# Optimization experiments

Measured on AMD Instinct MI355X. Metric: run time of the kernel, lower is better.

Reference implementation:

```python
import jax, jax.numpy as jnp
import numpy as np

N, C, H, W = 4, 256, 64, 64
K, G, PAD, STRIDE, DIL = 3, 8, 1, 1, 1
GC = C // G      # channels per group
P = K * K        # sampling points per group
HIN, WIN = H + 2 * PAD, W + 2 * PAD
BN_EPS = 1e-5
LN_EPS = 1e-5


def setup_inputs():
    key = jax.random.key(0)
    ks = jax.random.split(key, 8)
    f32 = jnp.float32
    return {
        "x": jax.random.normal(ks[0], (N, C, H, W), dtype=f32),
        "w_in": jax.random.normal(ks[1], (C, C), dtype=f32) * 0.05,
        "b_in": jnp.zeros((C,), f32),
        "w_dw": jax.random.normal(ks[2], (C, 1, K, K), dtype=f32) * 0.1,
        "b_dw": jnp.zeros((C,), f32),
        "ln_g": jnp.ones((C,), f32), "ln_b": jnp.zeros((C,), f32),
        "w_off": jax.random.normal(ks[3], (C, G * P * 2), dtype=f32) * 0.01,
        "b_off": jax.random.normal(ks[4], (G * P * 2,), dtype=f32) * 0.01,
        "w_mask": jax.random.normal(ks[5], (C, G * P), dtype=f32) * 0.01,
        "b_mask": jnp.zeros((G * P,), f32),
        "w_out": jax.random.normal(ks[6], (C, C), dtype=f32) * 0.05,
        "b_out": jnp.zeros((C,), f32),
        "bn_g": jnp.ones((C,), f32), "bn_b": jnp.zeros((C,), f32),
        "bn_mean": jnp.zeros((C,), f32), "bn_var": jnp.ones((C,), f32),
    }


def _bilinear(img, grid):
    # img: (B, Cc, Hh, Ww); grid: (B, S, P, 2) normalized to [-1,1],
    # matches F.grid_sample(mode='bilinear', padding_mode='zeros', align_corners=False)
    B, Cc, Hh, Ww = img.shape
    gx = (grid[..., 0] + 1.0) * 0.5 * Ww - 0.5
    gy = (grid[..., 1] + 1.0) * 0.5 * Hh - 0.5
    x0 = jnp.floor(gx)
    y0 = jnp.floor(gy)
    wx = gx - x0
    wy = gy - y0
    flat = img.reshape(B, Cc, Hh * Ww)

    def tap(xi, yi, wgt):
        valid = (xi >= 0) & (xi <= Ww - 1) & (yi >= 0) & (yi <= Hh - 1)
        idx = (jnp.clip(yi, 0, Hh - 1) * Ww + jnp.clip(xi, 0, Ww - 1)).astype(jnp.int32)
        v = jax.vmap(lambda im, ix: im[:, ix])(flat, idx)   # (B, Cc, S, P)
        return v * (wgt * valid.astype(img.dtype))[:, None]

    return (tap(x0, y0, (1 - wx) * (1 - wy)) + tap(x0 + 1, y0, wx * (1 - wy))
            + tap(x0, y0 + 1, (1 - wx) * wy) + tap(x0 + 1, y0 + 1, wx * wy))


def _forward(x, w_in, b_in, w_dw, b_dw, ln_g, ln_b, w_off, b_off,
             w_mask, b_mask, w_out, b_out, bn_g, bn_b, bn_mean, bn_var):
    xl = jnp.transpose(x, (0, 2, 3, 1))                      # (N,H,W,C) channels-last
    x_proj = xl @ w_in + b_in                                # input_proj
    # depthwise conv + LayerNorm + GELU feature branch for offset/mask prediction
    dw = jax.lax.conv_general_dilated(
        x, w_dw, (1, 1), ((PAD, PAD), (PAD, PAD)),
        feature_group_count=C, dimension_numbers=("NCHW", "OIHW", "NCHW"))
    dw = jnp.transpose(dw + b_dw[None, :, None, None], (0, 2, 3, 1))
    mu = dw.mean(-1, keepdims=True)
    var = ((dw - mu) ** 2).mean(-1, keepdims=True)
    dw = (dw - mu) * jax.lax.rsqrt(var + LN_EPS) * ln_g + ln_b
    x1 = jax.nn.gelu(dw, approximate=False)
    offset = x1 @ w_off + b_off                              # (N,H,W,G*P*2)
    mask = jax.nn.softmax((x1 @ w_mask + b_mask).reshape(N, H, W, G, P), axis=-1)
    # reference points + dilation kernel grid, normalized to padded input, (x,y) order
    ry = ((DIL * (K - 1)) // 2 + 0.5 + jnp.arange(H, dtype=x.dtype) * STRIDE) / HIN
    rx = ((DIL * (K - 1)) // 2 + 0.5 + jnp.arange(W, dtype=x.dtype) * STRIDE) / WIN
    ref = jnp.stack(jnp.broadcast_arrays(rx[None, :], ry[:, None]), axis=-1)  # (H,W,2)
    px = (jnp.arange(K, dtype=x.dtype) * DIL - (DIL * (K - 1)) // 2) / WIN
    py = (jnp.arange(K, dtype=x.dtype) * DIL - (DIL * (K - 1)) // 2) / HIN
    gx, gy = jnp.meshgrid(px, py, indexing="ij")             # kw-major flattening as in DCNv3
    kgrid = jnp.stack([gx, gy], -1).reshape(P, 2)
    norm = jnp.array([WIN, HIN], dtype=x.dtype)
    loc = (ref[None, :, :, None, None, :] + kgrid[None, None, None, None, :, :]
           + offset.reshape(N, H, W, G, P, 2) / norm)        # (N,H,W,G,P,2), offset_scale=1
    sgrid = 2.0 * loc - 1.0
    # group-split padded value tensor and deformable sampling
    xp = jnp.pad(x_proj, ((0, 0), (PAD, PAD), (PAD, PAD), (0, 0)))
    img = jnp.transpose(xp, (0, 3, 1, 2)).reshape(N * G, GC, HIN, WIN)
    sg = jnp.transpose(sgrid.reshape(N, H * W, G, P, 2), (0, 2, 1, 3, 4)).reshape(N * G, H * W, P, 2)
    sampled = _bilinear(img, sg)                             # (N*G, GC, H*W, P)
    m = jnp.transpose(mask.reshape(N, H * W, G, P), (0, 2, 1, 3)).reshape(N * G, 1, H * W, P)
    agg = (sampled * m).sum(-1)                              # (N*G, GC, H*W)
    y = jnp.transpose(agg.reshape(N, C, H * W), (0, 2, 1)).reshape(N, H, W, C)
    y = y @ w_out + b_out                                    # output_proj
    y = jnp.transpose(y, (0, 3, 1, 2))                       # back to NCHW
    y = (y - bn_mean[None, :, None, None]) * jax.lax.rsqrt(bn_var + BN_EPS)[None, :, None, None]
    y = y * bn_g[None, :, None, None] + bn_b[None, :, None, None]
    return y * jax.nn.sigmoid(y)                             # SiLU (Conv.default_act)


def reference(x, w_in, b_in, w_dw, b_dw, ln_g, ln_b, w_off, b_off,
              w_mask, b_mask, w_out, b_out, bn_g, bn_b, bn_mean, bn_var):
    return _forward(x, w_in, b_in, w_dw, b_dw, ln_g, ln_b, w_off, b_off,
                    w_mask, b_mask, w_out, b_out, bn_g, bn_b, bn_mean, bn_var)
```

## Files before the change

### kernel.cpp

```cpp
#include <hip/hip_runtime.h>
#include <math.h>

#define NB   4
#define CCH  256
#define HH   64
#define WW   64
#define GG   8
#define GCH  32
#define PP   9
#define HIN  66
#define WIN  66
#define HWSZ 4096
#define NPIX 16384

#define X16_ELEMS  (NPIX*CCH)
#define XP_ELEMS   (NB*HIN*WIN*CCH)
#define X1_ELEMS   (NPIX*CCH)
#define AGG_ELEMS  (NPIX*CCH)
#define WINT_ELEMS (CCH*CCH)
#define WOUTT_ELEMS (CCH*CCH)
#define WOMT_ELEMS (216*CCH)
#define OFF_ELEMS  (NPIX*144)
#define MSK_ELEMS  (NPIX*72)

typedef __attribute__((ext_vector_type(8))) short bf16x8;
typedef __attribute__((ext_vector_type(4))) float f32x4;

__device__ __forceinline__ unsigned short f2bf(float f) {
    unsigned int u = __float_as_uint(f);
    unsigned int r = (u + 0x7FFFu + ((u >> 16) & 1u)) >> 16;
    return (unsigned short)r;
}
__device__ __forceinline__ float bf2f(unsigned short s) {
    return __uint_as_float(((unsigned int)s) << 16);
}

#define SDW_STRIDE 258

__global__ __launch_bounds__(1024) void k_dw_prep(
    const float* __restrict__ x, const float* __restrict__ w_dw,
    const float* __restrict__ b_dw, const float* __restrict__ ln_g,
    const float* __restrict__ ln_b, const float* __restrict__ w_in,
    const float* __restrict__ w_off, const float* __restrict__ w_mask,
    const float* __restrict__ w_out, unsigned short* __restrict__ x1,
    unsigned short* __restrict__ x16, unsigned short* __restrict__ win_t,
    unsigned short* __restrict__ womt, unsigned short* __restrict__ wout_t,
    unsigned short* __restrict__ xp)
{
    const int b = blockIdx.x;
    const int tid = threadIdx.x;

    if (b >= 256) {
        const int gtid = (b - 256) * 1024 + tid;
        const int STRIDE = 34 * 1024;
        for (int i = gtid; i < 252928; i += STRIDE) {
            if (i < 65536) {
                int n = i & 255, k = i >> 8;
                win_t[n * 256 + k] = f2bf(w_in[i]);
            } else if (i < 131072) {
                int j = i - 65536;
                int n = j & 255, k = j >> 8;
                wout_t[n * 256 + k] = f2bf(w_out[j]);
            } else if (i < 186368) {
                int j = i - 131072;
                int k = j / 216, col = j - k * 216;
                float v = (col < 144) ? w_off[k * 144 + col]
                                      : w_mask[k * 72 + col - 144];
                womt[col * 256 + k] = f2bf(v);
            } else {
                int r = i - 186368;
                int seg = r >> 6, ln = r & 63;
                int n = seg / 260, rp = seg % 260;
                int h, w;
                if (rp < 66)       { h = 0;        w = rp; }
                else if (rp < 132) { h = 65;       w = rp - 66; }
                else if (rp < 196) { h = rp - 131; w = 0; }
                else               { h = rp - 195; w = 65; }
                uint2 z = make_uint2(0u, 0u);
                *(uint2*)&xp[(((size_t)n * HIN + h) * WIN + w) * CCH + ln * 4] = z;
            }
        }
        return;
    }

    __shared__ unsigned short sdw[64 * SDW_STRIDE];
    __shared__ unsigned short sxr[64 * SDW_STRIDE];
    __shared__ float r1s[16][64];
    __shared__ float r2s[16][64];
    __shared__ float mu_s[64];
    __shared__ float rs_s[64];

    const int h = b & 63;
    const int n = b >> 6;
    const int wave = tid >> 6;
    const int lane = tid & 63;

    const float* xn = x + (size_t)n * CCH * HWSZ;
    const bool h0ok = (h > 0);
    const bool h2ok = (h < HH - 1);

    float s1 = 0.f, s2 = 0.f;

#pragma unroll 4
    for (int it = 0; it < 16; it++) {
        const int c = it * 16 + wave;
        const float* xc = xn + (size_t)c * HWSZ + h * WW + lane;
        float v0 = h0ok ? xc[-WW] : 0.f;
        float v1 = xc[0];
        float v2 = h2ok ? xc[WW] : 0.f;

        const float* wk = w_dw + c * 9;
        float acc = b_dw[c];

        float l0 = __shfl_up(v0, 1);   if (lane == 0)  l0 = 0.f;
        float r0 = __shfl_down(v0, 1); if (lane == 63) r0 = 0.f;
        acc += wk[0] * l0 + wk[1] * v0 + wk[2] * r0;

        float l1 = __shfl_up(v1, 1);   if (lane == 0)  l1 = 0.f;
        float r1 = __shfl_down(v1, 1); if (lane == 63) r1 = 0.f;
        acc += wk[3] * l1 + wk[4] * v1 + wk[5] * r1;

        float l2 = __shfl_up(v2, 1);   if (lane == 0)  l2 = 0.f;
        float r2 = __shfl_down(v2, 1); if (lane == 63) r2 = 0.f;
        acc += wk[6] * l2 + wk[7] * v2 + wk[8] * r2;

        s1 += acc;
        s2 += acc * acc;
        sdw[lane * SDW_STRIDE + c] = f2bf(acc);
        sxr[lane * SDW_STRIDE + c] = f2bf(v1);
    }

    r1s[wave][lane] = s1;
    r2s[wave][lane] = s2;
    __syncthreads();

    if (tid < 64) {
        float a1 = 0.f, a2 = 0.f;
#pragma unroll
        for (int q = 0; q < 16; q++) { a1 += r1s[q][tid]; a2 += r2s[q][tid]; }
        float mu = a1 * (1.0f / 256.0f);
        float var = a2 * (1.0f / 256.0f) - mu * mu;
        mu_s[tid] = mu;
        rs_s[tid] = rsqrtf(var + 1e-5f);
    }
    __syncthreads();

    const int c0 = (tid & 63) * 4;
    const int wq = tid >> 6;
    float g4[4], b4[4];
#pragma unroll
    for (int i = 0; i < 4; i++) { g4[i] = ln_g[c0 + i]; b4[i] = ln_b[c0 + i]; }

    unsigned short* x1p  = x1  + (((size_t)n * HH + h) * WW) * CCH + c0;
    unsigned short* x16p = x16 + (((size_t)n * HH + h) * WW) * CCH + c0;
#pragma unroll
    for (int pass = 0; pass < 4; pass++) {
        int w = wq + pass * 16;
        float mu = mu_s[w], rs = rs_s[w];
        const unsigned short* row  = &sdw[w * SDW_STRIDE + c0];
        const unsigned short* rowx = &sxr[w * SDW_STRIDE + c0];
        unsigned short tmp[4];
#pragma unroll
        for (int i = 0; i < 4; i++) {
            float v = (bf2f(row[i]) - mu) * rs * g4[i] + b4[i];
            tmp[i] = f2bf(0.5f * v * (1.0f + erff(v * 0.70710678118654752f)));
        }
        ushort4 o; o.x = tmp[0]; o.y = tmp[1]; o.z = tmp[2]; o.w = tmp[3];
        *(ushort4*)&x1p[(size_t)w * CCH] = o;
        ushort4 xo; xo.x = rowx[0]; xo.y = rowx[1]; xo.z = rowx[2]; xo.w = rowx[3];
        *(ushort4*)&x16p[(size_t)w * CCH] = xo;
    }
}

__global__ __launch_bounds__(256) void k_proj(
    const unsigned short* __restrict__ x16, const unsigned short* __restrict__ win_t,
    const float* __restrict__ b_in, unsigned short* __restrict__ xp,
    const unsigned short* __restrict__ x1, const unsigned short* __restrict__ womt,
    const float* __restrict__ b_off, const float* __restrict__ b_mask,
    float* __restrict__ off, float* __restrict__ msk)
{
    const int b = blockIdx.x;
    const int tid = threadIdx.x;
    const int wave = tid >> 6;
    const int lane = tid & 63;
    const int r16  = lane & 15;
    const int quad = lane >> 4;
    const int mw   = wave * 32;

    f32x4 acc[2][4];
#pragma unroll
    for (int i = 0; i < 2; i++)
#pragma unroll
        for (int j = 0; j < 4; j++) acc[i][j] = (f32x4){0.f, 0.f, 0.f, 0.f};

    if (b < 512) {
        const int m0  = (b & 127) * 128;
        const int co0 = (b >> 7) * 64;
        const int n   = m0 >> 12;
        const int hw0 = m0 & 4095;

        const unsigned short* a0p = x16 + (size_t)(m0 + mw + r16) * CCH + quad * 8;
        const unsigned short* a1p = a0p + 16 * CCH;

#pragma unroll
        for (int k0 = 0; k0 < CCH; k0 += 32) {
            bf16x8 a0 = *(const bf16x8*)&a0p[k0];
            bf16x8 a1 = *(const bf16x8*)&a1p[k0];
#pragma unroll
            for (int nt = 0; nt < 4; nt++) {
                bf16x8 bfr = *(const bf16x8*)&win_t[(size_t)(co0 + nt * 16 + r16) * CCH + k0 + quad * 8];
                acc[0][nt] = __builtin_amdgcn_mfma_f32_16x16x32_bf16(a0, bfr, acc[0][nt], 0, 0, 0);
                acc[1][nt] = __builtin_amdgcn_mfma_f32_16x16x32_bf16(a1, bfr, acc[1][nt], 0, 0, 0);
            }
        }

#pragma unroll
        for (int nt = 0; nt < 4; nt++) {
            int co = co0 + nt * 16 + r16;
            float bias = b_in[co];
#pragma unroll
            for (int mt = 0; mt < 2; mt++) {
                int mbase = mw + mt * 16 + quad * 4;
#pragma unroll
                for (int r = 0; r < 4; r++) {
                    int hw = hw0 + mbase + r;
                    int h = hw >> 6, w = hw & 63;
                    xp[(((size_t)n * HIN + (h + 1)) * WIN + (w + 1)) * CCH + co] =
                        f2bf(acc[mt][nt][r] + bias);
                }
            }
        }
    } else {
        const int b2 = b - 512;
        const int m0  = (b2 & 127) * 128;
        const int co0 = (b2 >> 7) * 64;

        const unsigned short* a0p = x1 + (size_t)(m0 + mw + r16) * CCH + quad * 8;
        const unsigned short* a1p = a0p + 16 * CCH;

#pragma unroll
        for (int k0 = 0; k0 < CCH; k0 += 32) {
            bf16x8 a0 = *(const bf16x8*)&a0p[k0];
            bf16x8 a1 = *(const bf16x8*)&a1p[k0];
#pragma unroll
            for (int nt = 0; nt < 4; nt++) {
                int col = co0 + nt * 16 + r16;
                int colc = (col < 216) ? col : 215;
                bf16x8 bfr = *(const bf16x8*)&womt[(size_t)colc * CCH + k0 + quad * 8];
                acc[0][nt] = __builtin_amdgcn_mfma_f32_16x16x32_bf16(a0, bfr, acc[0][nt], 0, 0, 0);
                acc[1][nt] = __builtin_amdgcn_mfma_f32_16x16x32_bf16(a1, bfr, acc[1][nt], 0, 0, 0);
            }
        }

#pragma unroll
        for (int nt = 0; nt < 4; nt++) {
            int col = co0 + nt * 16 + r16;
            if (col >= 216) continue;
            float bias = (col < 144) ? b_off[col] : b_mask[col - 144];
#pragma unroll
            for (int mt = 0; mt < 2; mt++) {
                int mbase = m0 + mw + mt * 16 + quad * 4;
#pragma unroll
                for (int r = 0; r < 4; r++) {
                    int p = mbase + r;
                    float v = acc[mt][nt][r] + bias;
                    if (col < 144) off[(size_t)p * 144 + col] = v;
                    else           msk[(size_t)p * 72 + col - 144] = v;
                }
            }
        }
    }
}

__device__ __forceinline__ void acc8_tap(float* a, uint4 vv, float wgt) {
    a[0] += wgt * __uint_as_float(vv.x << 16);
    a[1] += wgt * __uint_as_float(vv.x & 0xffff0000u);
    a[2] += wgt * __uint_as_float(vv.y << 16);
    a[3] += wgt * __uint_as_float(vv.y & 0xffff0000u);
    a[4] += wgt * __uint_as_float(vv.z << 16);
    a[5] += wgt * __uint_as_float(vv.z & 0xffff0000u);
    a[6] += wgt * __uint_as_float(vv.w << 16);
    a[7] += wgt * __uint_as_float(vv.w & 0xffff0000u);
}

__global__ __launch_bounds__(256) void k_sample_agg(
    const unsigned short* __restrict__ xp, const float* __restrict__ off,
    const float* __restrict__ msk, unsigned short* __restrict__ agg)
{
    __shared__ float  sm[576];
    __shared__ int2   tco[576];
    __shared__ float4 twt[576];

    const int tid = threadIdx.x;
    const int s0 = blockIdx.x * 8;

    if (tid < 64) {
        const int pix = tid >> 3, g = tid & 7;
        const float* mskp = msk + (size_t)(s0 + pix) * 72 + g * 9;
        float e[9];
        float mx = -1e30f;
#pragma unroll
        for (int p = 0; p < PP; p++) { e[p] = mskp[p]; mx = fmaxf(mx, e[p]); }
        float sum = 0.f;
#pragma unroll
        for (int p = 0; p < PP; p++) { e[p] = __expf(e[p] - mx); sum += e[p]; }
        float rs = 1.0f / sum;
#pragma unroll
        for (int p = 0; p < PP; p++) sm[tid * 9 + p] = e[p] * rs;
    }
    __syncthreads();

    for (int idx = tid; idx < 576; idx += 256) {
        int pix = idx / 72;
        int rem = idx - pix * 72;
        int g = rem / 9;
        int p = rem - g * 9;
        int s = s0 + pix;
        int hw = s & 4095;
        int h = hw >> 6, w = hw & 63;
        const float* offp = off + (size_t)s * 144 + g * 18 + p * 2;
        float ox = offp[0], oy = offp[1];
        int i = p / 3, j = p - i * 3;
        float fx = (float)(w + i) + ox;
        float fy = (float)(h + j) + oy;
        float x0f = floorf(fx), y0f = floorf(fy);
        int x0 = (int)x0f, y0 = (int)y0f;
        float wx = fx - x0f, wy = fy - y0f;
        float m = sm[idx];
        float w00 = (1.f - wx) * (1.f - wy) * m;
        float w10 = wx * (1.f - wy) * m;
        float w01 = (1.f - wx) * wy * m;
        float w11 = wx * wy * m;
        int x1c = x0 + 1, y1c = y0 + 1;
        if (!((x0  >= 0) && (x0  < WIN))) { w00 = 0.f; w01 = 0.f; }
        if (!((x1c >= 0) && (x1c < WIN))) { w10 = 0.f; w11 = 0.f; }
        if (!((y0  >= 0) && (y0  < HIN))) { w00 = 0.f; w10 = 0.f; }
        if (!((y1c >= 0) && (y1c < HIN))) { w01 = 0.f; w11 = 0.f; }
        int cx0 = min(max(x0, 0), WIN - 1), cx1 = min(max(x1c, 0), WIN - 1);
        int cy0 = min(max(y0, 0), HIN - 1), cy1 = min(max(y1c, 0), HIN - 1);
        tco[idx] = make_int2(cx0 | (cx1 << 16), cy0 | (cy1 << 16));
        twt[idx] = make_float4(w00, w10, w01, w11);
    }
    __syncthreads();

    const int pix = tid >> 5;
    const int l5 = tid & 31;
    const int g = l5 >> 2, c8 = l5 & 3;
    const int s = s0 + pix;
    const int n = s >> 12;
    const unsigned short* base = xp + (size_t)n * HIN * WIN * CCH + g * GCH + c8 * 8;
    const int tbase = pix * 72 + g * 9;

    float a[8];
#pragma unroll
    for (int i = 0; i < 8; i++) a[i] = 0.f;

#pragma unroll
    for (int p = 0; p < PP; p++) {
        int2 cc = tco[tbase + p];
        float4 wt = twt[tbase + p];
        int cx0 = cc.x & 0xFFFF, cx1 = cc.x >> 16;
        int cy0 = cc.y & 0xFFFF, cy1 = cc.y >> 16;
        const unsigned short* r0 = base + (size_t)(cy0 * WIN) * CCH;
        const unsigned short* r1 = base + (size_t)(cy1 * WIN) * CCH;
        uint4 v00 = *(const uint4*)&r0[(size_t)cx0 * CCH];
        uint4 v10 = *(const uint4*)&r0[(size_t)cx1 * CCH];
        uint4 v01 = *(const uint4*)&r1[(size_t)cx0 * CCH];
        uint4 v11 = *(const uint4*)&r1[(size_t)cx1 * CCH];
        acc8_tap(a, v00, wt.x);
        acc8_tap(a, v10, wt.y);
        acc8_tap(a, v01, wt.z);
        acc8_tap(a, v11, wt.w);
    }

    uint4 o;
    o.x = (unsigned int)f2bf(a[0]) | ((unsigned int)f2bf(a[1]) << 16);
    o.y = (unsigned int)f2bf(a[2]) | ((unsigned int)f2bf(a[3]) << 16);
    o.z = (unsigned int)f2bf(a[4]) | ((unsigned int)f2bf(a[5]) << 16);
    o.w = (unsigned int)f2bf(a[6]) | ((unsigned int)f2bf(a[7]) << 16);
    *(uint4*)&agg[(size_t)s * CCH + g * GCH + c8 * 8] = o;
}

__global__ __launch_bounds__(256) void k_gemm_out(
    const unsigned short* __restrict__ agg, const unsigned short* __restrict__ wout_t,
    const float* __restrict__ b_out, const float* __restrict__ bn_g,
    const float* __restrict__ bn_b, const float* __restrict__ bn_mean,
    const float* __restrict__ bn_var, float* __restrict__ out)
{
    const int m0  = blockIdx.x * 128;
    const int co0 = blockIdx.y * 64;
    const int tid = threadIdx.x;
    const int n   = m0 >> 12;
    const int hw0 = m0 & 4095;

    const int wave = tid >> 6;
    const int lane = tid & 63;
    const int r16  = lane & 15;
    const int quad = lane >> 4;
    const int mw   = wave * 32;

    f32x4 acc[2][4];
#pragma unroll
    for (int i = 0; i < 2; i++)
#pragma unroll
        for (int j = 0; j < 4; j++) acc[i][j] = (f32x4){0.f, 0.f, 0.f, 0.f};

    const unsigned short* a0p = agg + (size_t)(m0 + mw + r16) * CCH + quad * 8;
    const unsigned short* a1p = a0p + 16 * CCH;

#pragma unroll
    for (int k0 = 0; k0 < CCH; k0 += 32) {
        bf16x8 a0 = *(const bf16x8*)&a0p[k0];
        bf16x8 a1 = *(const bf16x8*)&a1p[k0];
#pragma unroll
        for (int nt = 0; nt < 4; nt++) {
            bf16x8 bfr = *(const bf16x8*)&wout_t[(size_t)(co0 + nt * 16 + r16) * CCH + k0 + quad * 8];
            acc[0][nt] = __builtin_amdgcn_mfma_f32_16x16x32_bf16(a0, bfr, acc[0][nt], 0, 0, 0);
            acc[1][nt] = __builtin_amdgcn_mfma_f32_16x16x32_bf16(a1, bfr, acc[1][nt], 0, 0, 0);
        }
    }

#pragma unroll
    for (int nt = 0; nt < 4; nt++) {
        int co = co0 + nt * 16 + r16;
        float mean = bn_mean[co];
        float rstd = rsqrtf(bn_var[co] + 1e-5f);
        float gg = bn_g[co], bb = bn_b[co], bo = b_out[co];
#pragma unroll
        for (int mt = 0; mt < 2; mt++) {
            int hwb = hw0 + mw + mt * 16 + quad * 4;
            float tmp[4];
#pragma unroll
            for (int r = 0; r < 4; r++) {
                float y = acc[mt][nt][r] + bo;
                float yh = (y - mean) * rstd * gg + bb;
                tmp[r] = yh / (1.0f + __expf(-yh));
            }
            float4 v = make_float4(tmp[0], tmp[1], tmp[2], tmp[3]);
            *(float4*)&out[((size_t)n * CCH + co) * HWSZ + hwb] = v;
        }
    }
}

extern "C" void kernel_launch(void* const* d_in, const int* in_sizes, int n_in,
                              void* d_out, int out_size, void* d_ws, size_t ws_size,
                              hipStream_t stream)
{
    const float* x       = (const float*)d_in[0];
    const float* w_in    = (const float*)d_in[1];
    const float* b_in    = (const float*)d_in[2];
    const float* w_dw    = (const float*)d_in[3];
    const float* b_dw    = (const float*)d_in[4];
    const float* ln_g    = (const float*)d_in[5];
    const float* ln_b    = (const float*)d_in[6];
    const float* w_off   = (const float*)d_in[7];
    const float* b_off   = (const float*)d_in[8];
    const float* w_mask  = (const float*)d_in[9];
    const float* b_mask  = (const float*)d_in[10];
    const float* w_out   = (const float*)d_in[11];
    const float* b_out   = (const float*)d_in[12];
    const float* bn_g    = (const float*)d_in[13];
    const float* bn_b    = (const float*)d_in[14];
    const float* bn_mean = (const float*)d_in[15];
    const float* bn_var  = (const float*)d_in[16];
    float* out = (float*)d_out;

    unsigned short* xp     = (unsigned short*)d_ws;
    unsigned short* x16    = xp + XP_ELEMS;
    unsigned short* x1     = x16 + X16_ELEMS;
    unsigned short* agg    = x1 + X1_ELEMS;
    unsigned short* win_t  = agg + AGG_ELEMS;
    unsigned short* wout_t = win_t + WINT_ELEMS;
    unsigned short* womt   = wout_t + WOUTT_ELEMS;
    float* off = (float*)(womt + WOMT_ELEMS);
    float* msk = off + OFF_ELEMS;

    k_dw_prep<<<dim3(290), 1024, 0, stream>>>(x, w_dw, b_dw, ln_g, ln_b,
                                              w_in, w_off, w_mask, w_out,
                                              x1, x16, win_t, womt, wout_t, xp);
    k_proj<<<dim3(1024), 256, 0, stream>>>(x16, win_t, b_in, xp,
                                           x1, womt, b_off, b_mask, off, msk);
    k_sample_agg<<<dim3(2048), 256, 0, stream>>>(xp, off, msk, agg);
    k_gemm_out<<<dim3(128, 4), 256, 0, stream>>>(agg, wout_t, b_out, bn_g, bn_b, bn_mean, bn_var, out);
}
```

Before: 176.2 us.

## Fuse input and offset/mask projections into depthwise kernel using LDS-resident rows

Splits weight conversion and border zeroing into a small separate kernel. The depthwise, LayerNorm and GELU stage then runs the input projection and the offset/mask projection GEMMs directly from its shared-memory rows. This removes the x16/x1 global round trip and the separate projection kernel launch. In exchange, the fused kernel has only 256 blocks of 1024 threads with 16 waves each computing 16x64 tiles, so parallelism is lower, weight B fragments are re-read from global per block, and LDS A-fragment loads are done as 32-bit reads.

Result: no change. 178.1 us (+1.1%).

```diff
diff --git a/kernel.cpp b/kernel.cpp
--- a/kernel.cpp
+++ b/kernel.cpp
@@ -13,9 +13,7 @@
 #define HWSZ 4096
 #define NPIX 16384
 
-#define X16_ELEMS  (NPIX*CCH)
 #define XP_ELEMS   (NB*HIN*WIN*CCH)
-#define X1_ELEMS   (NPIX*CCH)
 #define AGG_ELEMS  (NPIX*CCH)
 #define WINT_ELEMS (CCH*CCH)
 #define WOUTT_ELEMS (CCH*CCH)
@@ -37,52 +35,52 @@
 
 #define SDW_STRIDE 258
 
-__global__ __launch_bounds__(1024) void k_dw_prep(
+__global__ __launch_bounds__(256) void k_prep(
+    const float* __restrict__ w_in, const float* __restrict__ w_off,
+    const float* __restrict__ w_mask, const float* __restrict__ w_out,
+    unsigned short* __restrict__ win_t, unsigned short* __restrict__ womt,
+    unsigned short* __restrict__ wout_t, unsigned short* __restrict__ xp)
+{
+    const int gtid = blockIdx.x * 256 + threadIdx.x;
+    const int STRIDE = 128 * 256;
+    for (int i = gtid; i < 252928; i += STRIDE) {
+        if (i < 65536) {
+            int n = i & 255, k = i >> 8;
+            win_t[n * 256 + k] = f2bf(w_in[i]);
+        } else if (i < 131072) {
+            int j = i - 65536;
+            int n = j & 255, k = j >> 8;
+            wout_t[n * 256 + k] = f2bf(w_out[j]);
+        } else if (i < 186368) {
+            int j = i - 131072;
+            int k = j / 216, col = j - k * 216;
+            float v = (col < 144) ? w_off[k * 144 + col]
+                                  : w_mask[k * 72 + col - 144];
+            womt[col * 256 + k] = f2bf(v);
+        } else {
+            int r = i - 186368;
+            int seg = r >> 6, ln = r & 63;
+            int n = seg / 260, rp = seg % 260;
+            int h, w;
+            if (rp < 66)       { h = 0;        w = rp; }
+            else if (rp < 132) { h = 65;       w = rp - 66; }
+            else if (rp < 196) { h = rp - 131; w = 0; }
+            else               { h = rp - 195; w = 65; }
+            uint2 z = make_uint2(0u, 0u);
+            *(uint2*)&xp[(((size_t)n * HIN + h) * WIN + w) * CCH + ln * 4] = z;
+        }
+    }
+}
+
+__global__ __launch_bounds__(1024) void k_dw_fused(
     const float* __restrict__ x, const float* __restrict__ w_dw,
     const float* __restrict__ b_dw, const float* __restrict__ ln_g,
-    const float* __restrict__ ln_b, const float* __restrict__ w_in,
-    const float* __restrict__ w_off, const float* __restrict__ w_mask,
-    const float* __restrict__ w_out, unsigned short* __restrict__ x1,
-    unsigned short* __restrict__ x16, unsigned short* __restrict__ win_t,
-    unsigned short* __restrict__ womt, unsigned short* __restrict__ wout_t,
-    unsigned short* __restrict__ xp)
+    const float* __restrict__ ln_b, const float* __restrict__ b_in,
+    const unsigned short* __restrict__ win_t, const unsigned short* __restrict__ womt,
+    const float* __restrict__ b_off, const float* __restrict__ b_mask,
+    unsigned short* __restrict__ xp, float* __restrict__ off,
+    float* __restrict__ msk)
 {
-    const int b = blockIdx.x;
-    const int tid = threadIdx.x;
-
-    if (b >= 256) {
-        const int gtid = (b - 256) * 1024 + tid;
-        const int STRIDE = 34 * 1024;
-        for (int i = gtid; i < 252928; i += STRIDE) {
-            if (i < 65536) {
-                int n = i & 255, k = i >> 8;
-                win_t[n * 256 + k] = f2bf(w_in[i]);
-            } else if (i < 131072) {
-                int j = i - 65536;
-                int n = j & 255, k = j >> 8;
-                wout_t[n * 256 + k] = f2bf(w_out[j]);
-            } else if (i < 186368) {
-                int j = i - 131072;
-                int k = j / 216, col = j - k * 216;
-                float v = (col < 144) ? w_off[k * 144 + col]
-                                      : w_mask[k * 72 + col - 144];
-                womt[col * 256 + k] = f2bf(v);
-            } else {
-                int r = i - 186368;
-                int seg = r >> 6, ln = r & 63;
-                int n = seg / 260, rp = seg % 260;
-                int h, w;
-                if (rp < 66)       { h = 0;        w = rp; }
-                else if (rp < 132) { h = 65;       w = rp - 66; }
-                else if (rp < 196) { h = rp - 131; w = 0; }
-                else               { h = rp - 195; w = 65; }
-                uint2 z = make_uint2(0u, 0u);
-                *(uint2*)&xp[(((size_t)n * HIN + h) * WIN + w) * CCH + ln * 4] = z;
-            }
-        }
-        return;
-    }
-
     __shared__ unsigned short sdw[64 * SDW_STRIDE];
     __shared__ unsigned short sxr[64 * SDW_STRIDE];
     __shared__ float r1s[16][64];
@@ -90,9 +88,11 @@
     __shared__ float mu_s[64];
     __shared__ float rs_s[64];
 
+    const int b = blockIdx.x;
+    const int tid = threadIdx.x;
     const int h = b & 63;
     const int n = b >> 6;
-    const int wave = tid >> 6;
+    const int wave = __builtin_amdgcn_readfirstlane(tid >> 6);
     const int lane = tid & 63;
 
     const float* xn = x + (size_t)n * CCH * HWSZ;
@@ -145,131 +145,106 @@
     }
     __syncthreads();
 
-    const int c0 = (tid & 63) * 4;
-    const int wq = tid >> 6;
-    float g4[4], b4[4];
-#pragma unroll
-    for (int i = 0; i < 4; i++) { g4[i] = ln_g[c0 + i]; b4[i] = ln_b[c0 + i]; }
-
-    unsigned short* x1p  = x1  + (((size_t)n * HH + h) * WW) * CCH + c0;
-    unsigned short* x16p = x16 + (((size_t)n * HH + h) * WW) * CCH + c0;
-#pragma unroll
-    for (int pass = 0; pass < 4; pass++) {
-        int w = wq + pass * 16;
-        float mu = mu_s[w], rs = rs_s[w];
-        const unsigned short* row  = &sdw[w * SDW_STRIDE + c0];
-        const unsigned short* rowx = &sxr[w * SDW_STRIDE + c0];
-        unsigned short tmp[4];
-#pragma unroll
-        for (int i = 0; i < 4; i++) {
-            float v = (bf2f(row[i]) - mu) * rs * g4[i] + b4[i];
-            tmp[i] = f2bf(0.5f * v * (1.0f + erff(v * 0.70710678118654752f)));
-        }
-        ushort4 o; o.x = tmp[0]; o.y = tmp[1]; o.z = tmp[2]; o.w = tmp[3];
-        *(ushort4*)&x1p[(size_t)w * CCH] = o;
-        ushort4 xo; xo.x = rowx[0]; xo.y = rowx[1]; xo.z = rowx[2]; xo.w = rowx[3];
-        *(ushort4*)&x16p[(size_t)w * CCH] = xo;
-    }
-}
-
-__global__ __launch_bounds__(256) void k_proj(
-    const unsigned short* __restrict__ x16, const unsigned short* __restrict__ win_t,
-    const float* __restrict__ b_in, unsigned short* __restrict__ xp,
-    const unsigned short* __restrict__ x1, const unsigned short* __restrict__ womt,
-    const float* __restrict__ b_off, const float* __restrict__ b_mask,
-    float* __restrict__ off, float* __restrict__ msk)
-{
-    const int b = blockIdx.x;
-    const int tid = threadIdx.x;
-    const int wave = tid >> 6;
-    const int lane = tid & 63;
+    {
+        const int c0 = (tid & 63) * 4;
+        float g4[4], b4[4];
+#pragma unroll
+        for (int i = 0; i < 4; i++) { g4[i] = ln_g[c0 + i]; b4[i] = ln_b[c0 + i]; }
+#pragma unroll
+        for (int pass = 0; pass < 4; pass++) {
+            int w = wave + pass * 16;
+            float mu = mu_s[w], rs = rs_s[w];
+            unsigned short* row = &sdw[w * SDW_STRIDE + c0];
+#pragma unroll
+            for (int i = 0; i < 4; i++) {
+                float v = (bf2f(row[i]) - mu) * rs * g4[i] + b4[i];
+                row[i] = f2bf(0.5f * v * (1.0f + erff(v * 0.70710678118654752f)));
+            }
+        }
+    }
+    __syncthreads();
+
     const int r16  = lane & 15;
     const int quad = lane >> 4;
-    const int mw   = wave * 32;
-
-    f32x4 acc[2][4];
-#pragma unroll
-    for (int i = 0; i < 2; i++)
-#pragma unroll
-        for (int j = 0; j < 4; j++) acc[i][j] = (f32x4){0.f, 0.f, 0.f, 0.f};
-
-    if (b < 512) {
-        const int m0  = (b & 127) * 128;
-        const int co0 = (b >> 7) * 64;
-        const int n   = m0 >> 12;
-        const int hw0 = m0 & 4095;
-
-        const unsigned short* a0p = x16 + (size_t)(m0 + mw + r16) * CCH + quad * 8;
-        const unsigned short* a1p = a0p + 16 * CCH;
+    const int wm   = wave >> 2;
+    const int wn   = wave & 3;
+
+#define LOAD_A(frag, basep, koff)                                   \
+    {                                                               \
+        const unsigned short* ap_ = (basep) + (koff);               \
+        ((unsigned int*)&(frag))[0] = *(const unsigned int*)&ap_[0];\
+        ((unsigned int*)&(frag))[1] = *(const unsigned int*)&ap_[2];\
+        ((unsigned int*)&(frag))[2] = *(const unsigned int*)&ap_[4];\
+        ((unsigned int*)&(frag))[3] = *(const unsigned int*)&ap_[6];\
+    }
+
+    {
+        f32x4 acc[4];
+#pragma unroll
+        for (int i = 0; i < 4; i++) acc[i] = (f32x4){0.f, 0.f, 0.f, 0.f};
+        const unsigned short* arow = &sxr[(wm * 16 + r16) * SDW_STRIDE];
 
 #pragma unroll
         for (int k0 = 0; k0 < CCH; k0 += 32) {
-            bf16x8 a0 = *(const bf16x8*)&a0p[k0];
-            bf16x8 a1 = *(const bf16x8*)&a1p[k0];
-#pragma unroll
-            for (int nt = 0; nt < 4; nt++) {
-                bf16x8 bfr = *(const bf16x8*)&win_t[(size_t)(co0 + nt * 16 + r16) * CCH + k0 + quad * 8];
-                acc[0][nt] = __builtin_amdgcn_mfma_f32_16x16x32_bf16(a0, bfr, acc[0][nt], 0, 0, 0);
-                acc[1][nt] = __builtin_amdgcn_mfma_f32_16x16x32_bf16(a1, bfr, acc[1][nt], 0, 0, 0);
-            }
-        }
-
-#pragma unroll
-        for (int nt = 0; nt < 4; nt++) {
-            int co = co0 + nt * 16 + r16;
+            bf16x8 a;
+            LOAD_A(a, arow, k0 + quad * 8);
+#pragma unroll
+            for (int i = 0; i < 4; i++) {
+                int co = (wn * 4 + i) * 16 + r16;
+                bf16x8 bfr = *(const bf16x8*)&win_t[(size_t)co * CCH + k0 + quad * 8];
+                acc[i] = __builtin_amdgcn_mfma_f32_16x16x32_bf16(a, bfr, acc[i], 0, 0, 0);
+            }
+        }
+
+        unsigned short* xprow = xp + (((size_t)n * HIN + (h + 1)) * WIN + 1) * CCH;
+#pragma unroll
+        for (int i = 0; i < 4; i++) {
+            int co = (wn * 4 + i) * 16 + r16;
             float bias = b_in[co];
 #pragma unroll
-            for (int mt = 0; mt < 2; mt++) {
-                int mbase = mw + mt * 16 + quad * 4;
-#pragma unroll
-                for (int r = 0; r < 4; r++) {
-                    int hw = hw0 + mbase + r;
-                    int h = hw >> 6, w = hw & 63;
-                    xp[(((size_t)n * HIN + (h + 1)) * WIN + (w + 1)) * CCH + co] =
-                        f2bf(acc[mt][nt][r] + bias);
-                }
-            }
-        }
-    } else {
-        const int b2 = b - 512;
-        const int m0  = (b2 & 127) * 128;
-        const int co0 = (b2 >> 7) * 64;
-
-        const unsigned short* a0p = x1 + (size_t)(m0 + mw + r16) * CCH + quad * 8;
-        const unsigned short* a1p = a0p + 16 * CCH;
+            for (int r = 0; r < 4; r++) {
+                int w = wm * 16 + quad * 4 + r;
+                xprow[(size_t)w * CCH + co] = f2bf(acc[i][r] + bias);
+            }
+        }
+    }
+
+    {
+        f32x4 acc[4];
+#pragma unroll
+        for (int i = 0; i < 4; i++) acc[i] = (f32x4){0.f, 0.f, 0.f, 0.f};
+        const unsigned short* arow = &sdw[(wm * 16 + r16) * SDW_STRIDE];
 
 #pragma unroll
         for (int k0 = 0; k0 < CCH; k0 += 32) {
-            bf16x8 a0 = *(const bf16x8*)&a0p[k0];
-            bf16x8 a1 = *(const bf16x8*)&a1p[k0];
-#pragma unroll
-            for (int nt = 0; nt < 4; nt++) {
-                int col = co0 + nt * 16 + r16;
+            bf16x8 a;
+            LOAD_A(a, arow, k0 + quad * 8);
+#pragma unroll
+            for (int i = 0; i < 4; i++) {
+                int col = (wn * 4 + i) * 16 + r16;
                 int colc = (col < 216) ? col : 215;
                 bf16x8 bfr = *(const bf16x8*)&womt[(size_t)colc * CCH + k0 + quad * 8];
-                acc[0][nt] = __builtin_amdgcn_mfma_f32_16x16x32_bf16(a0, bfr, acc[0][nt], 0, 0, 0);
-                acc[1][nt] = __builtin_amdgcn_mfma_f32_16x16x32_bf16(a1, bfr, acc[1][nt], 0, 0, 0);
-            }
-        }
-
-#pragma unroll
-        for (int nt = 0; nt < 4; nt++) {
-            int col = co0 + nt * 16 + r16;
+                acc[i] = __builtin_amdgcn_mfma_f32_16x16x32_bf16(a, bfr, acc[i], 0, 0, 0);
+            }
+        }
+
+        const int sbase = n * HWSZ + h * WW;
+#pragma unroll
+        for (int i = 0; i < 4; i++) {
+            int col = (wn * 4 + i) * 16 + r16;
             if (col >= 216) continue;
             float bias = (col < 144) ? b_off[col] : b_mask[col - 144];
 #pragma unroll
-            for (int mt = 0; mt < 2; mt++) {
-                int mbase = m0 + mw + mt * 16 + quad * 4;
-#pragma unroll
-                for (int r = 0; r < 4; r++) {
-                    int p = mbase + r;
-                    float v = acc[mt][nt][r] + bias;
-                    if (col < 144) off[(size_t)p * 144 + col] = v;
-                    else           msk[(size_t)p * 72 + col - 144] = v;
-                }
-            }
-        }
-    }
+            for (int r = 0; r < 4; r++) {
+                int w = wm * 16 + quad * 4 + r;
+                int s = sbase + w;
+                float v = acc[i][r] + bias;
+                if (col < 144) off[(size_t)s * 144 + col] = v;
+                else           msk[(size_t)s * 72 + col - 144] = v;
+            }
+        }
+    }
+#undef LOAD_A
 }
 
 __device__ __forceinline__ void acc8_tap(float* a, uint4 vv, float wgt) {
@@ -466,20 +441,18 @@
     float* out = (float*)d_out;
 
     unsigned short* xp     = (unsigned short*)d_ws;
-    unsigned short* x16    = xp + XP_ELEMS;
-    unsigned short* x1     = x16 + X16_ELEMS;
-    unsigned short* agg    = x1 + X1_ELEMS;
+    unsigned short* agg    = xp + XP_ELEMS;
     unsigned short* win_t  = agg + AGG_ELEMS;
     unsigned short* wout_t = win_t + WINT_ELEMS;
     unsigned short* womt   = wout_t + WOUTT_ELEMS;
     float* off = (float*)(womt + WOMT_ELEMS);
     float* msk = off + OFF_ELEMS;
 
-    k_dw_prep<<<dim3(290), 1024, 0, stream>>>(x, w_dw, b_dw, ln_g, ln_b,
-                                              w_in, w_off, w_mask, w_out,
-                                              x1, x16, win_t, womt, wout_t, xp);
-    k_proj<<<dim3(1024), 256, 0, stream>>>(x16, win_t, b_in, xp,
-                                           x1, womt, b_off, b_mask, off, msk);
+    k_prep<<<dim3(128), 256, 0, stream>>>(w_in, w_off, w_mask, w_out,
+                                          win_t, womt, wout_t, xp);
+    k_dw_fused<<<dim3(256), 1024, 0, stream>>>(x, w_dw, b_dw, ln_g, ln_b, b_in,
+                                               win_t, womt, b_off, b_mask,
+                                               xp, off, msk);
     k_sample_agg<<<dim3(2048), 256, 0, stream>>>(xp, off, msk, agg);
     k_gemm_out<<<dim3(128, 4), 256, 0, stream>>>(agg, wout_t, b_out, bn_g, bn_b, bn_mean, bn_var, out);
 }
```
